# Kernel optimization log

Hardware: AMD Instinct MI355X
Metric: run time of the kernel (lower is better)

Reference implementation:

```python
import jax, jax.numpy as jnp
from jax import lax
import numpy as np

B, S, H = 8, 512, 768


def setup_inputs() -> dict:
    key = jax.random.key(0)
    ks = jax.random.split(key, 8)
    outputs = jax.random.normal(ks[0], (B, S, H), dtype=jnp.float32)
    starts = jax.random.randint(ks[1], (B,), S // 4, 3 * S // 4)
    mask = jnp.stack([starts, jnp.full((B,), S, dtype=starts.dtype)], axis=1)  # [B,2]
    sc = 1.0 / np.sqrt(H)
    Wa_w = jax.random.normal(ks[2], (H, H), dtype=jnp.float32) * sc
    Wa_b = jax.random.normal(ks[3], (H,), dtype=jnp.float32) * sc
    Ua_w = jax.random.normal(ks[4], (H, H), dtype=jnp.float32) * sc
    Ua_b = jax.random.normal(ks[5], (H,), dtype=jnp.float32) * sc
    Va_w = jax.random.normal(ks[6], (1, H), dtype=jnp.float32) * sc
    Va_b = jax.random.normal(ks[7], (1,), dtype=jnp.float32) * sc
    return {"outputs": outputs, "mask": mask, "Wa_w": Wa_w, "Wa_b": Wa_b,
            "Ua_w": Ua_w, "Ua_b": Ua_b, "Va_w": Va_w, "Va_b": Va_b}


def reference(outputs, mask, Wa_w, Wa_b, Ua_w, Ua_b, Va_w, Va_b):
    # outputs: [B,S,H]; mask[:,0] = start (source = tokens [0:start], summary = [start:S])
    b, s, h = outputs.shape
    Wq = jnp.einsum('bsh,oh->bso', outputs, Wa_w) + Wa_b  # query proj, [B,S,H]
    Uk = jnp.einsum('bsh,oh->bso', outputs, Ua_w) + Ua_b  # key proj,   [B,S,H]
    va = Va_w[0]  # [H]
    vb = Va_b[0]

    # Stream over query token positions to avoid a [B,S,S,H] tanh intermediate.
    def step(_, wq_t):  # wq_t: [B,H]
        m = jnp.tanh(wq_t[:, None, :] + Uk)          # [B,S,H]
        sc_t = jnp.einsum('bkh,h->bk', m, va) + vb   # [B,S]
        return None, sc_t

    _, scores = lax.scan(step, None, jnp.swapaxes(Wq, 0, 1))  # [S(query token), B, S(key)]
    scores = jnp.swapaxes(scores, 0, 1)  # [B, S_token, S_key]

    start = mask[:, 0]                              # [B]
    j = jnp.arange(s)
    # summary query j corresponds to token index start + j
    t_idx = jnp.clip(start[:, None] + j[None, :], 0, s - 1)            # [B,S]
    sc = jnp.take_along_axis(scores, t_idx[:, :, None], axis=1)       # [B,S,S]
    key_mask = (j[None, :] < start[:, None])                           # [B,S] valid source keys
    q_mask = (j[None, :] < (s - start)[:, None])                       # [B,S] valid summary queries

    sc = jnp.where(key_mask[:, None, :], sc, -1e30)
    w = jax.nn.softmax(sc, axis=-1)
    # zero out exactly where the torch code leaves zeros
    attentions = w * key_mask[:, None, :].astype(w.dtype) * q_mask[:, :, None].astype(w.dtype)
    contexts = jnp.einsum('bjk,bkh->bjh', attentions, outputs)
    return attentions, contexts
```

## Files before the change

### kernel.cpp

```cpp
#include <hip/hip_runtime.h>

typedef float  f32x4   __attribute__((ext_vector_type(4)));
typedef short  short8  __attribute__((ext_vector_type(8)));
typedef unsigned short ushort8 __attribute__((ext_vector_type(8)));

constexpr int kB = 8;
constexpr int kS = 512;
constexpr int kH = 768;
constexpr int kJM = 384;

constexpr float kTanhScale = 2.8853900817779268f;

__device__ __forceinline__ float native_exp2(float x) {
    float r; asm("v_exp_f32 %0, %1" : "=v"(r) : "v"(x)); return r;
}

__device__ __forceinline__ float waveMax(float v) {
#pragma unroll
    for (int off = 32; off > 0; off >>= 1) v = fmaxf(v, __shfl_xor(v, off, 64));
    return v;
}
__device__ __forceinline__ float waveSum(float v) {
#pragma unroll
    for (int off = 32; off > 0; off >>= 1) v += __shfl_xor(v, off, 64);
    return v;
}

__global__ __launch_bounds__(256) void k0_convert(
    const float* __restrict__ X, const float* __restrict__ Wa, const float* __restrict__ Ua,
    unsigned short* __restrict__ Xhi, unsigned short* __restrict__ Xlo,
    unsigned short* __restrict__ Wahi, unsigned short* __restrict__ Walo,
    unsigned short* __restrict__ Uahi, unsigned short* __restrict__ Ualo)
{
    const int i4 = blockIdx.x * 256 + threadIdx.x;
    const float* src; unsigned short *hi, *lo; int off;
    if (i4 < 786432)      { src = X;  hi = Xhi;  lo = Xlo;  off = i4; }
    else if (i4 < 933888) { src = Wa; hi = Wahi; lo = Walo; off = i4 - 786432; }
    else                  { src = Ua; hi = Uahi; lo = Ualo; off = i4 - 933888; }

    float4 v = *(const float4*)(src + (size_t)off * 4);
    unsigned short h[4], l[4];
#pragma unroll
    for (int c = 0; c < 4; ++c) {
        float x = (&v.x)[c];
        unsigned u = __float_as_uint(x);
        h[c] = (unsigned short)(u >> 16);
        float hf = __uint_as_float(u & 0xFFFF0000u);
        l[c] = (unsigned short)(__float_as_uint(x - hf) >> 16);
    }
    *(ushort4*)(hi + (size_t)off * 4) = make_ushort4(h[0], h[1], h[2], h[3]);
    *(ushort4*)(lo + (size_t)off * 4) = make_ushort4(l[0], l[1], l[2], l[3]);
}

__global__ __launch_bounds__(256) void k1_mfma(
    const unsigned short* __restrict__ Xhi, const unsigned short* __restrict__ Xlo,
    const unsigned short* __restrict__ W0hi, const unsigned short* __restrict__ W0lo,
    const unsigned short* __restrict__ W1hi, const unsigned short* __restrict__ W1lo,
    const float* __restrict__ b0, const float* __restrict__ b1,
    const int* __restrict__ mask,
    float* __restrict__ Eqc, float* __restrict__ EkTc)
{
    __shared__ char smem[49664];
    unsigned short* Ahi = (unsigned short*)smem;
    unsigned short* Alo = (unsigned short*)(smem + 10240);
    unsigned short* Bhi = (unsigned short*)(smem + 20480);
    unsigned short* Blo = (unsigned short*)(smem + 28160);

    const int z = blockIdx.z;
    const unsigned short* Whi = z ? W1hi : W0hi;
    const unsigned short* Wlo = z ? W1lo : W0lo;
    const float* bias = z ? b1 : b0;

    const int m0 = blockIdx.y * 128;
    const int n0 = blockIdx.x * 96;
    const int t  = threadIdx.x;
    const int bI = m0 >> 9;
    const int lb = m0 & (kS - 1);
    const int start = mask[2 * bI];

    if (z == 0) { if (lb + 128 <= start) return; }
    else        { if (lb >= start) return; }

    const int ar = t >> 1, ko = (t & 1) << 4;
    const bool doB = (ar < 96);
    const size_t aoff = (size_t)(m0 + ar) * kH + ko;
    const size_t woff = (size_t)(n0 + ar) * kH + ko;

    const int wid = t >> 6, lane = t & 63;
    const int wr = wid >> 1, wc = wid & 1;
    const int lr = lane & 15, lk = (lane >> 4) << 3;

    f32x4 acc[4][3];
#pragma unroll
    for (int mi = 0; mi < 4; ++mi)
#pragma unroll
        for (int ni = 0; ni < 3; ++ni)
#pragma unroll
            for (int r = 0; r < 4; ++r) acc[mi][ni][r] = 0.0f;

    for (int h0 = 0; h0 < kH; h0 += 32) {
        ushort8 ah0 = *(const ushort8*)(Xhi + aoff + h0);
        ushort8 ah1 = *(const ushort8*)(Xhi + aoff + h0 + 8);
        ushort8 al0 = *(const ushort8*)(Xlo + aoff + h0);
        ushort8 al1 = *(const ushort8*)(Xlo + aoff + h0 + 8);
        ushort8 bh0, bh1, bl0, bl1;
        if (doB) {
            bh0 = *(const ushort8*)(Whi + woff + h0);
            bh1 = *(const ushort8*)(Whi + woff + h0 + 8);
            bl0 = *(const ushort8*)(Wlo + woff + h0);
            bl1 = *(const ushort8*)(Wlo + woff + h0 + 8);
        }
        __syncthreads();
        *(ushort8*)(Ahi + ar * 40 + ko)     = ah0;
        *(ushort8*)(Ahi + ar * 40 + ko + 8) = ah1;
        *(ushort8*)(Alo + ar * 40 + ko)     = al0;
        *(ushort8*)(Alo + ar * 40 + ko + 8) = al1;
        if (doB) {
            *(ushort8*)(Bhi + ar * 40 + ko)     = bh0;
            *(ushort8*)(Bhi + ar * 40 + ko + 8) = bh1;
            *(ushort8*)(Blo + ar * 40 + ko)     = bl0;
            *(ushort8*)(Blo + ar * 40 + ko + 8) = bl1;
        }
        __syncthreads();

        short8 ah[4], al_[4], bh[3], bl[3];
#pragma unroll
        for (int mi = 0; mi < 4; ++mi) {
            const int row = wr * 64 + mi * 16 + lr;
            ah[mi]  = *(const short8*)(Ahi + row * 40 + lk);
            al_[mi] = *(const short8*)(Alo + row * 40 + lk);
        }
#pragma unroll
        for (int ni = 0; ni < 3; ++ni) {
            const int row = wc * 48 + ni * 16 + lr;
            bh[ni] = *(const short8*)(Bhi + row * 40 + lk);
            bl[ni] = *(const short8*)(Blo + row * 40 + lk);
        }
#pragma unroll
        for (int mi = 0; mi < 4; ++mi)
#pragma unroll
            for (int ni = 0; ni < 3; ++ni)
                acc[mi][ni] = __builtin_amdgcn_mfma_f32_16x16x32_bf16(ah[mi], bh[ni], acc[mi][ni], 0, 0, 0);
#pragma unroll
        for (int mi = 0; mi < 4; ++mi)
#pragma unroll
            for (int ni = 0; ni < 3; ++ni)
                acc[mi][ni] = __builtin_amdgcn_mfma_f32_16x16x32_bf16(al_[mi], bh[ni], acc[mi][ni], 0, 0, 0);
#pragma unroll
        for (int mi = 0; mi < 4; ++mi)
#pragma unroll
            for (int ni = 0; ni < 3; ++ni)
                acc[mi][ni] = __builtin_amdgcn_mfma_f32_16x16x32_bf16(ah[mi], bl[ni], acc[mi][ni], 0, 0, 0);
    }

    if (z == 0) {
#pragma unroll
        for (int mi = 0; mi < 4; ++mi)
#pragma unroll
            for (int ni = 0; ni < 3; ++ni) {
                const int ml = lb + wr * 64 + mi * 16 + ((lane >> 4) << 2);
                const int ng = n0 + wc * 48 + ni * 16 + lr;
                const float bn = bias[ng];
#pragma unroll
                for (int r = 0; r < 4; ++r) {
                    const int jj = ml + r - start;
                    if (jj >= 0)
                        Eqc[((size_t)bI * kJM + jj) * kH + ng] =
                            native_exp2((acc[mi][ni][r] + bn) * kTanhScale);
                }
            }
    } else {
        __syncthreads();
        float* stg = (float*)smem;
#pragma unroll
        for (int mi = 0; mi < 4; ++mi)
#pragma unroll
            for (int ni = 0; ni < 3; ++ni) {
                const int ml = wr * 64 + mi * 16 + ((lane >> 4) << 2);
                const int nl = wc * 48 + ni * 16 + lr;
                const float bn = bias[n0 + nl];
#pragma unroll
                for (int r = 0; r < 4; ++r)
                    stg[(ml + r) * 97 + nl] = native_exp2((acc[mi][ni][r] + bn) * kTanhScale);
            }
        __syncthreads();
        const int s4 = (t & 31) << 2, hb_ = t >> 5;
        const int sg = lb + s4;
#pragma unroll
        for (int u = 0; u < 12; ++u) {
            const int h = (u << 3) + hb_;
            float o[4] = { stg[(s4 + 0) * 97 + h], stg[(s4 + 1) * 97 + h],
                           stg[(s4 + 2) * 97 + h], stg[(s4 + 3) * 97 + h] };
            float* dst = EkTc + ((size_t)bI * kH + n0 + h) * kJM + sg;
            if (sg + 3 < start) {
                *(float4*)dst = make_float4(o[0], o[1], o[2], o[3]);
            } else {
#pragma unroll
                for (int e2 = 0; e2 < 4; ++e2)
                    if (sg + e2 < start) dst[e2] = o[e2];
            }
        }
    }
}

__global__ void k2a_worklist(const int* __restrict__ mask, int* __restrict__ wl)
{
    __shared__ int ne[kB], off[kB];
    const int tid = threadIdx.x;
    if (tid < kB) {
        int start = mask[2 * tid];
        ne[tid] = ((kS - start + 1) >> 1) * ((start + 63) >> 6) * 2;
    }
    __syncthreads();
    if (tid == 0) {
        int s = 0;
        for (int b = 0; b < kB; ++b) { off[b] = s; s += ne[b]; }
        wl[0] = s;
    }
    __syncthreads();
    for (int b = 0; b < kB; ++b) {
        int start = mask[2 * b];
        int nkw = (start + 63) >> 6;
        int n = ne[b], base = off[b];
        for (int t = tid; t < n; t += blockDim.x) {
            int c = t & 1, p = t >> 1;
            int jt = p / nkw, kt = p - jt * nkw;
            wl[1 + base + t] = (b << 16) | (jt << 8) | (kt << 1) | c;
        }
    }
}

__global__ __launch_bounds__(256) void k2_scores(
    const float* __restrict__ Eqc, const float* __restrict__ EkTc,
    const float* __restrict__ va, const int* __restrict__ mask,
    const int* __restrict__ wl, float* __restrict__ part0, float* __restrict__ part1)
{
    const int ntiles = wl[0];
    const int lane = threadIdx.x & 63;
    const int wslot = (blockIdx.x << 2) | (threadIdx.x >> 6);
    const int nslots = gridDim.x << 2;

    for (int w = wslot; w < ntiles; w += nslots) {
        const int e = __builtin_amdgcn_readfirstlane(wl[1 + w]);
        const int b = e >> 16, jt = (e >> 8) & 255, ktc = e & 255;
        const int kt = ktc >> 1, c = ktc & 1;
        const int start = __builtin_amdgcn_readfirstlane(mask[2 * b]);
        const int jmax = kS - start;
        const int j0 = jt << 1, k0 = kt << 6;
        const int hbase = c * 384;

        const float* eq0 = Eqc + ((size_t)b * kJM + j0) * kH + hbase;
        const float* eq1 = eq0 + kH;
        const float* ekp = EkTc + ((size_t)b * kH + hbase) * kJM + k0 + lane;
        const float* vap = va + hbase;

        float a0 = 0.0f, a1 = 0.0f;
        float eA[8], eB[8];
#pragma unroll
        for (int c2 = 0; c2 < 8; ++c2) eA[c2] = ekp[(size_t)c2 * kJM];
#pragma unroll
        for (int c2 = 0; c2 < 8; ++c2) eB[c2] = ekp[(size_t)(8 + c2) * kJM];

        for (int h0 = 0; h0 < 384; h0 += 16) {
            const bool more = (h0 + 16) < 384;
            float nA[8], nB[8];
            if (more) {
#pragma unroll
                for (int c2 = 0; c2 < 8; ++c2) nA[c2] = ekp[(size_t)(h0 + 16 + c2) * kJM];
            }
#pragma unroll
            for (int c2 = 0; c2 < 8; ++c2) {
                const float vc = vap[h0 + c2];
                float r0 = __builtin_amdgcn_rcpf(fmaf(eq0[h0 + c2], eA[c2], 1.0f));
                float r1 = __builtin_amdgcn_rcpf(fmaf(eq1[h0 + c2], eA[c2], 1.0f));
                a0 = fmaf(vc, r0, a0);
                a1 = fmaf(vc, r1, a1);
            }
            if (more) {
#pragma unroll
                for (int c2 = 0; c2 < 8; ++c2) nB[c2] = ekp[(size_t)(h0 + 24 + c2) * kJM];
#pragma unroll
                for (int c2 = 0; c2 < 8; ++c2) {
                    const float vc = vap[h0 + 8 + c2];
                    float r0 = __builtin_amdgcn_rcpf(fmaf(eq0[h0 + 8 + c2], eB[c2], 1.0f));
                    float r1 = __builtin_amdgcn_rcpf(fmaf(eq1[h0 + 8 + c2], eB[c2], 1.0f));
                    a0 = fmaf(vc, r0, a0);
                    a1 = fmaf(vc, r1, a1);
                }
#pragma unroll
                for (int c2 = 0; c2 < 8; ++c2) { eA[c2] = nA[c2]; eB[c2] = nB[c2]; }
            } else {
#pragma unroll
                for (int c2 = 0; c2 < 8; ++c2) {
                    const float vc = vap[h0 + 8 + c2];
                    float r0 = __builtin_amdgcn_rcpf(fmaf(eq0[h0 + 8 + c2], eB[c2], 1.0f));
                    float r1 = __builtin_amdgcn_rcpf(fmaf(eq1[h0 + 8 + c2], eB[c2], 1.0f));
                    a0 = fmaf(vc, r0, a0);
                    a1 = fmaf(vc, r1, a1);
                }
            }
        }

        float* srow = (c ? part1 : part0) + ((size_t)b * kS + j0) * kS + k0 + lane;
        if (j0 < jmax)     srow[0]  = -2.0f * a0;
        if (j0 + 1 < jmax) srow[kS] = -2.0f * a1;
    }
}

__global__ __launch_bounds__(256) void k3_softmax(
    float* __restrict__ attn, const float* __restrict__ part1,
    const int* __restrict__ mask)
{
    const int bx = blockIdx.x;
    const int b = bx >> 9;
    const int j = bx & (kS - 1);
    const int start = mask[2 * b];
    float* row = attn + ((size_t)b * kS + j) * kS;
    const int tid = threadIdx.x;

    if (j >= kS - start) {
        row[tid] = 0.0f;
        row[tid + 256] = 0.0f;
        return;
    }

    const float* p1row = part1 + ((size_t)b * kS + j) * kS;
    float v0 = (tid < start) ? row[tid] + p1row[tid] : -1e30f;
    float v1 = (tid + 256 < start) ? row[tid + 256] + p1row[tid + 256] : -1e30f;

    __shared__ float red[4];
    const int wid = tid >> 6;

    float m = waveMax(fmaxf(v0, v1));
    if ((tid & 63) == 0) red[wid] = m;
    __syncthreads();
    m = fmaxf(fmaxf(red[0], red[1]), fmaxf(red[2], red[3]));
    __syncthreads();

    float e0 = (tid < start) ? __expf(v0 - m) : 0.0f;
    float e1 = (tid + 256 < start) ? __expf(v1 - m) : 0.0f;
    float s = waveSum(e0 + e1);
    if ((tid & 63) == 0) red[wid] = s;
    __syncthreads();
    s = red[0] + red[1] + red[2] + red[3];

    float inv = __builtin_amdgcn_rcpf(s);
    row[tid] = e0 * inv;
    row[tid + 256] = e1 * inv;
}

__global__ __launch_bounds__(256) void k4_context(
    const float* __restrict__ attn, const float* __restrict__ outs,
    const int* __restrict__ mask, float* __restrict__ ctx)
{
    const int b = blockIdx.z;
    const int start = mask[2 * b];
    const int kmax = (start + 15) & ~15;
    const int m0 = blockIdx.y * 64;
    const int n0 = blockIdx.x * 64;

    __shared__ float As[16][68];
    __shared__ float Bs[16][68];

    const int tid = threadIdx.x;
    const int lrow = tid >> 2;
    const int lk4  = (tid & 3) << 2;
    const int brow = tid >> 4;
    const int bh4  = (tid & 15) << 2;
    const int is = tid >> 4;
    const int js = tid & 15;

    const float* arow = attn + ((size_t)b * kS + m0 + lrow) * kS + lk4;
    const float* bbase = outs + (size_t)b * kS * kH + n0 + bh4;

    float acc[4][4] = {};

    for (int k0 = 0; k0 < kmax; k0 += 16) {
        float4 av = *(const float4*)(arow + k0);
        float4 bv = *(const float4*)(bbase + (size_t)(k0 + brow) * kH);
        __syncthreads();
        As[lk4 + 0][lrow] = av.x;
        As[lk4 + 1][lrow] = av.y;
        As[lk4 + 2][lrow] = av.z;
        As[lk4 + 3][lrow] = av.w;
        *(float4*)&Bs[brow][bh4] = bv;
        __syncthreads();
#pragma unroll
        for (int kk = 0; kk < 16; ++kk) {
            const float* ap = &As[kk][is << 2];
            const float* bp = &Bs[kk][js << 2];
            float aa[4], bb[4];
#pragma unroll
            for (int c = 0; c < 4; ++c) { aa[c] = ap[c]; bb[c] = bp[c]; }
#pragma unroll
            for (int i = 0; i < 4; ++i)
#pragma unroll
                for (int j = 0; j < 4; ++j)
                    acc[i][j] = fmaf(aa[i], bb[j], acc[i][j]);
        }
    }

#pragma unroll
    for (int i = 0; i < 4; ++i) {
        int row = m0 + (is << 2) + i;
        float4 o = {acc[i][0], acc[i][1], acc[i][2], acc[i][3]};
        *(float4*)(ctx + ((size_t)b * kS + row) * kH + n0 + (js << 2)) = o;
    }
}

extern "C" void kernel_launch(void* const* d_in, const int* in_sizes, int n_in,
                              void* d_out, int out_size, void* d_ws, size_t ws_size,
                              hipStream_t stream)
{
    const float* outputs = (const float*)d_in[0];
    const int*   mask    = (const int*)d_in[1];
    const float* Wa_w    = (const float*)d_in[2];
    const float* Wa_b    = (const float*)d_in[3];
    const float* Ua_w    = (const float*)d_in[4];
    const float* Ua_b    = (const float*)d_in[5];
    const float* Va_w    = (const float*)d_in[6];

    float* attn = (float*)d_out;
    float* ctx  = attn + (size_t)kB * kS * kS;

    unsigned short* Xhi  = (unsigned short*)ctx;
    unsigned short* Xlo  = Xhi + (size_t)kB * kS * kH;
    unsigned short* Wahi = (unsigned short*)attn;
    unsigned short* Walo = Wahi + (size_t)kH * kH;
    unsigned short* Uahi = Walo + (size_t)kH * kH;
    unsigned short* Ualo = Uahi + (size_t)kH * kH;
    float* part1 = ctx;

    int* wl = (int*)d_ws;
    float* Eqc  = (float*)((char*)d_ws + 131072);
    float* EkTc = Eqc + (size_t)kB * kJM * kH;

    k0_convert<<<dim3(4224), 256, 0, stream>>>(
        outputs, Wa_w, Ua_w, Xhi, Xlo, Wahi, Walo, Uahi, Ualo);

    k1_mfma<<<dim3(kH / 96, (kB * kS) / 128, 2), 256, 0, stream>>>(
        Xhi, Xlo, Wahi, Walo, Uahi, Ualo, Wa_b, Ua_b, mask, Eqc, EkTc);

    k2a_worklist<<<dim3(1), 256, 0, stream>>>(mask, wl);
    k2_scores<<<dim3(2048), 256, 0, stream>>>(Eqc, EkTc, Va_w, mask, wl, attn, part1);

    k3_softmax<<<dim3(kB * kS), 256, 0, stream>>>(attn, part1, mask);

    k4_context<<<dim3(kH / 64, kS / 64, kB), 256, 0, stream>>>(attn, outputs, mask, ctx);
}
```

Before: 152.0 us.

## Drop weight lo split, inline worklist decode, and pack score math into float2

The weights are now converted to a single bfloat16 with round-to-nearest, and only the activations keep a hi/lo split. This removes a third of the MFMAs and the weight-lo loads and LDS traffic in the projection GEMM, at some cost in accuracy. The separate worklist kernel is removed; each wave decodes its tile index from per-batch offsets computed from the mask, saving one launch. The scores inner loop uses 2-wide vector FMAs so the compiler can emit packed float ops.

```diff
diff --git a/kernel.cpp b/kernel.cpp
--- a/kernel.cpp
+++ b/kernel.cpp
@@ -1,6 +1,7 @@
 #include <hip/hip_runtime.h>
 
 typedef float  f32x4   __attribute__((ext_vector_type(4)));
+typedef float  v2f     __attribute__((ext_vector_type(2)));
 typedef short  short8  __attribute__((ext_vector_type(8)));
 typedef unsigned short ushort8 __attribute__((ext_vector_type(8)));
 
@@ -15,6 +16,12 @@
     float r; asm("v_exp_f32 %0, %1" : "=v"(r) : "v"(x)); return r;
 }
 
+__device__ __forceinline__ unsigned short bf16_rtn(float x) {
+    unsigned u = __float_as_uint(x);
+    unsigned r = u + 0x7FFFu + ((u >> 16) & 1u);
+    return (unsigned short)(r >> 16);
+}
+
 __device__ __forceinline__ float waveMax(float v) {
 #pragma unroll
     for (int off = 32; off > 0; off >>= 1) v = fmaxf(v, __shfl_xor(v, off, 64));
@@ -29,33 +36,34 @@
 __global__ __launch_bounds__(256) void k0_convert(
     const float* __restrict__ X, const float* __restrict__ Wa, const float* __restrict__ Ua,
     unsigned short* __restrict__ Xhi, unsigned short* __restrict__ Xlo,
-    unsigned short* __restrict__ Wahi, unsigned short* __restrict__ Walo,
-    unsigned short* __restrict__ Uahi, unsigned short* __restrict__ Ualo)
+    unsigned short* __restrict__ Wahi, unsigned short* __restrict__ Uahi)
 {
     const int i4 = blockIdx.x * 256 + threadIdx.x;
-    const float* src; unsigned short *hi, *lo; int off;
-    if (i4 < 786432)      { src = X;  hi = Xhi;  lo = Xlo;  off = i4; }
-    else if (i4 < 933888) { src = Wa; hi = Wahi; lo = Walo; off = i4 - 786432; }
-    else                  { src = Ua; hi = Uahi; lo = Ualo; off = i4 - 933888; }
-
-    float4 v = *(const float4*)(src + (size_t)off * 4);
-    unsigned short h[4], l[4];
-#pragma unroll
-    for (int c = 0; c < 4; ++c) {
-        float x = (&v.x)[c];
-        unsigned u = __float_as_uint(x);
-        h[c] = (unsigned short)(u >> 16);
-        float hf = __uint_as_float(u & 0xFFFF0000u);
-        l[c] = (unsigned short)(__float_as_uint(x - hf) >> 16);
-    }
-    *(ushort4*)(hi + (size_t)off * 4) = make_ushort4(h[0], h[1], h[2], h[3]);
-    *(ushort4*)(lo + (size_t)off * 4) = make_ushort4(l[0], l[1], l[2], l[3]);
+    if (i4 < 786432) {
+        float4 v = *(const float4*)(X + (size_t)i4 * 4);
+        unsigned short h[4], l[4];
+#pragma unroll
+        for (int c = 0; c < 4; ++c) {
+            float x = (&v.x)[c];
+            h[c] = bf16_rtn(x);
+            float hf = __uint_as_float((unsigned)h[c] << 16);
+            l[c] = bf16_rtn(x - hf);
+        }
+        *(ushort4*)(Xhi + (size_t)i4 * 4) = make_ushort4(h[0], h[1], h[2], h[3]);
+        *(ushort4*)(Xlo + (size_t)i4 * 4) = make_ushort4(l[0], l[1], l[2], l[3]);
+    } else {
+        const float* src; unsigned short* hi; int off;
+        if (i4 < 933888) { src = Wa; hi = Wahi; off = i4 - 786432; }
+        else             { src = Ua; hi = Uahi; off = i4 - 933888; }
+        float4 v = *(const float4*)(src + (size_t)off * 4);
+        *(ushort4*)(hi + (size_t)off * 4) =
+            make_ushort4(bf16_rtn(v.x), bf16_rtn(v.y), bf16_rtn(v.z), bf16_rtn(v.w));
+    }
 }
 
 __global__ __launch_bounds__(256) void k1_mfma(
     const unsigned short* __restrict__ Xhi, const unsigned short* __restrict__ Xlo,
-    const unsigned short* __restrict__ W0hi, const unsigned short* __restrict__ W0lo,
-    const unsigned short* __restrict__ W1hi, const unsigned short* __restrict__ W1lo,
+    const unsigned short* __restrict__ W0hi, const unsigned short* __restrict__ W1hi,
     const float* __restrict__ b0, const float* __restrict__ b1,
     const int* __restrict__ mask,
     float* __restrict__ Eqc, float* __restrict__ EkTc)
@@ -64,11 +72,9 @@
     unsigned short* Ahi = (unsigned short*)smem;
     unsigned short* Alo = (unsigned short*)(smem + 10240);
     unsigned short* Bhi = (unsigned short*)(smem + 20480);
-    unsigned short* Blo = (unsigned short*)(smem + 28160);
 
     const int z = blockIdx.z;
     const unsigned short* Whi = z ? W1hi : W0hi;
-    const unsigned short* Wlo = z ? W1lo : W0lo;
     const float* bias = z ? b1 : b0;
 
     const int m0 = blockIdx.y * 128;
@@ -103,12 +109,10 @@
         ushort8 ah1 = *(const ushort8*)(Xhi + aoff + h0 + 8);
         ushort8 al0 = *(const ushort8*)(Xlo + aoff + h0);
         ushort8 al1 = *(const ushort8*)(Xlo + aoff + h0 + 8);
-        ushort8 bh0, bh1, bl0, bl1;
+        ushort8 bh0, bh1;
         if (doB) {
             bh0 = *(const ushort8*)(Whi + woff + h0);
             bh1 = *(const ushort8*)(Whi + woff + h0 + 8);
-            bl0 = *(const ushort8*)(Wlo + woff + h0);
-            bl1 = *(const ushort8*)(Wlo + woff + h0 + 8);
         }
         __syncthreads();
         *(ushort8*)(Ahi + ar * 40 + ko)     = ah0;
@@ -118,12 +122,10 @@
         if (doB) {
             *(ushort8*)(Bhi + ar * 40 + ko)     = bh0;
             *(ushort8*)(Bhi + ar * 40 + ko + 8) = bh1;
-            *(ushort8*)(Blo + ar * 40 + ko)     = bl0;
-            *(ushort8*)(Blo + ar * 40 + ko + 8) = bl1;
-        }
-        __syncthreads();
-
-        short8 ah[4], al_[4], bh[3], bl[3];
+        }
+        __syncthreads();
+
+        short8 ah[4], al_[4], bh[3];
 #pragma unroll
         for (int mi = 0; mi < 4; ++mi) {
             const int row = wr * 64 + mi * 16 + lr;
@@ -134,7 +136,6 @@
         for (int ni = 0; ni < 3; ++ni) {
             const int row = wc * 48 + ni * 16 + lr;
             bh[ni] = *(const short8*)(Bhi + row * 40 + lk);
-            bl[ni] = *(const short8*)(Blo + row * 40 + lk);
         }
 #pragma unroll
         for (int mi = 0; mi < 4; ++mi)
@@ -146,11 +147,6 @@
 #pragma unroll
             for (int ni = 0; ni < 3; ++ni)
                 acc[mi][ni] = __builtin_amdgcn_mfma_f32_16x16x32_bf16(al_[mi], bh[ni], acc[mi][ni], 0, 0, 0);
-#pragma unroll
-        for (int mi = 0; mi < 4; ++mi)
-#pragma unroll
-            for (int ni = 0; ni < 3; ++ni)
-                acc[mi][ni] = __builtin_amdgcn_mfma_f32_16x16x32_bf16(ah[mi], bl[ni], acc[mi][ni], 0, 0, 0);
     }
 
     if (z == 0) {
@@ -203,49 +199,38 @@
     }
 }
 
-__global__ void k2a_worklist(const int* __restrict__ mask, int* __restrict__ wl)
-{
-    __shared__ int ne[kB], off[kB];
-    const int tid = threadIdx.x;
-    if (tid < kB) {
-        int start = mask[2 * tid];
-        ne[tid] = ((kS - start + 1) >> 1) * ((start + 63) >> 6) * 2;
-    }
-    __syncthreads();
-    if (tid == 0) {
-        int s = 0;
-        for (int b = 0; b < kB; ++b) { off[b] = s; s += ne[b]; }
-        wl[0] = s;
-    }
-    __syncthreads();
-    for (int b = 0; b < kB; ++b) {
-        int start = mask[2 * b];
-        int nkw = (start + 63) >> 6;
-        int n = ne[b], base = off[b];
-        for (int t = tid; t < n; t += blockDim.x) {
-            int c = t & 1, p = t >> 1;
-            int jt = p / nkw, kt = p - jt * nkw;
-            wl[1 + base + t] = (b << 16) | (jt << 8) | (kt << 1) | c;
-        }
-    }
-}
-
 __global__ __launch_bounds__(256) void k2_scores(
     const float* __restrict__ Eqc, const float* __restrict__ EkTc,
     const float* __restrict__ va, const int* __restrict__ mask,
-    const int* __restrict__ wl, float* __restrict__ part0, float* __restrict__ part1)
-{
-    const int ntiles = wl[0];
+    float* __restrict__ part0, float* __restrict__ part1)
+{
     const int lane = threadIdx.x & 63;
     const int wslot = (blockIdx.x << 2) | (threadIdx.x >> 6);
     const int nslots = gridDim.x << 2;
 
+    int starts[kB], offs[kB + 1];
+    offs[0] = 0;
+#pragma unroll
+    for (int b = 0; b < kB; ++b) {
+        int s = __builtin_amdgcn_readfirstlane(mask[2 * b]);
+        starts[b] = s;
+        offs[b + 1] = offs[b] + ((kS - s + 1) >> 1) * ((s + 63) >> 6) * 2;
+    }
+    const int ntiles = offs[kB];
+    const v2f one2 = {1.0f, 1.0f};
+
     for (int w = wslot; w < ntiles; w += nslots) {
-        const int e = __builtin_amdgcn_readfirstlane(wl[1 + w]);
-        const int b = e >> 16, jt = (e >> 8) & 255, ktc = e & 255;
-        const int kt = ktc >> 1, c = ktc & 1;
-        const int start = __builtin_amdgcn_readfirstlane(mask[2 * b]);
+        int b = 0;
+#pragma unroll
+        for (int i = 1; i < kB; ++i) b += (w >= offs[i]);
+        const int start = starts[b];
         const int jmax = kS - start;
+        const int tt = w - offs[b];
+        const int c = tt & 1;
+        const int p = tt >> 1;
+        const int nkw = (start + 63) >> 6;
+        const int jt = p / nkw;
+        const int kt = p - jt * nkw;
         const int j0 = jt << 1, k0 = kt << 6;
         const int hbase = c * 384;
 
@@ -254,7 +239,7 @@
         const float* ekp = EkTc + ((size_t)b * kH + hbase) * kJM + k0 + lane;
         const float* vap = va + hbase;
 
-        float a0 = 0.0f, a1 = 0.0f;
+        v2f acc0 = {0.0f, 0.0f}, acc1 = {0.0f, 0.0f};
         float eA[8], eB[8];
 #pragma unroll
         for (int c2 = 0; c2 < 8; ++c2) eA[c2] = ekp[(size_t)c2 * kJM];
@@ -269,41 +254,44 @@
                 for (int c2 = 0; c2 < 8; ++c2) nA[c2] = ekp[(size_t)(h0 + 16 + c2) * kJM];
             }
 #pragma unroll
-            for (int c2 = 0; c2 < 8; ++c2) {
-                const float vc = vap[h0 + c2];
-                float r0 = __builtin_amdgcn_rcpf(fmaf(eq0[h0 + c2], eA[c2], 1.0f));
-                float r1 = __builtin_amdgcn_rcpf(fmaf(eq1[h0 + c2], eA[c2], 1.0f));
-                a0 = fmaf(vc, r0, a0);
-                a1 = fmaf(vc, r1, a1);
+            for (int c2 = 0; c2 < 8; c2 += 2) {
+                v2f eq0p = *(const v2f*)(eq0 + h0 + c2);
+                v2f eq1p = *(const v2f*)(eq1 + h0 + c2);
+                v2f vap2 = *(const v2f*)(vap + h0 + c2);
+                v2f ek2 = {eA[c2], eA[c2 + 1]};
+                v2f p0 = __builtin_elementwise_fma(eq0p, ek2, one2);
+                v2f p1 = __builtin_elementwise_fma(eq1p, ek2, one2);
+                v2f r0 = {__builtin_amdgcn_rcpf(p0.x), __builtin_amdgcn_rcpf(p0.y)};
+                v2f r1 = {__builtin_amdgcn_rcpf(p1.x), __builtin_amdgcn_rcpf(p1.y)};
+                acc0 = __builtin_elementwise_fma(vap2, r0, acc0);
+                acc1 = __builtin_elementwise_fma(vap2, r1, acc1);
             }
             if (more) {
 #pragma unroll
                 for (int c2 = 0; c2 < 8; ++c2) nB[c2] = ekp[(size_t)(h0 + 24 + c2) * kJM];
-#pragma unroll
-                for (int c2 = 0; c2 < 8; ++c2) {
-                    const float vc = vap[h0 + 8 + c2];
-                    float r0 = __builtin_amdgcn_rcpf(fmaf(eq0[h0 + 8 + c2], eB[c2], 1.0f));
-                    float r1 = __builtin_amdgcn_rcpf(fmaf(eq1[h0 + 8 + c2], eB[c2], 1.0f));
-                    a0 = fmaf(vc, r0, a0);
-                    a1 = fmaf(vc, r1, a1);
-                }
+            }
+#pragma unroll
+            for (int c2 = 0; c2 < 8; c2 += 2) {
+                v2f eq0p = *(const v2f*)(eq0 + h0 + 8 + c2);
+                v2f eq1p = *(const v2f*)(eq1 + h0 + 8 + c2);
+                v2f vap2 = *(const v2f*)(vap + h0 + 8 + c2);
+                v2f ek2 = {eB[c2], eB[c2 + 1]};
+                v2f p0 = __builtin_elementwise_fma(eq0p, ek2, one2);
+                v2f p1 = __builtin_elementwise_fma(eq1p, ek2, one2);
+                v2f r0 = {__builtin_amdgcn_rcpf(p0.x), __builtin_amdgcn_rcpf(p0.y)};
+                v2f r1 = {__builtin_amdgcn_rcpf(p1.x), __builtin_amdgcn_rcpf(p1.y)};
+                acc0 = __builtin_elementwise_fma(vap2, r0, acc0);
+                acc1 = __builtin_elementwise_fma(vap2, r1, acc1);
+            }
+            if (more) {
 #pragma unroll
                 for (int c2 = 0; c2 < 8; ++c2) { eA[c2] = nA[c2]; eB[c2] = nB[c2]; }
-            } else {
-#pragma unroll
-                for (int c2 = 0; c2 < 8; ++c2) {
-                    const float vc = vap[h0 + 8 + c2];
-                    float r0 = __builtin_amdgcn_rcpf(fmaf(eq0[h0 + 8 + c2], eB[c2], 1.0f));
-                    float r1 = __builtin_amdgcn_rcpf(fmaf(eq1[h0 + 8 + c2], eB[c2], 1.0f));
-                    a0 = fmaf(vc, r0, a0);
-                    a1 = fmaf(vc, r1, a1);
-                }
             }
         }
 
         float* srow = (c ? part1 : part0) + ((size_t)b * kS + j0) * kS + k0 + lane;
-        if (j0 < jmax)     srow[0]  = -2.0f * a0;
-        if (j0 + 1 < jmax) srow[kS] = -2.0f * a1;
+        if (j0 < jmax)     srow[0]  = -2.0f * (acc0.x + acc0.y);
+        if (j0 + 1 < jmax) srow[kS] = -2.0f * (acc1.x + acc1.y);
     }
 }
 
@@ -426,23 +414,19 @@
     unsigned short* Xhi  = (unsigned short*)ctx;
     unsigned short* Xlo  = Xhi + (size_t)kB * kS * kH;
     unsigned short* Wahi = (unsigned short*)attn;
-    unsigned short* Walo = Wahi + (size_t)kH * kH;
-    unsigned short* Uahi = Walo + (size_t)kH * kH;
-    unsigned short* Ualo = Uahi + (size_t)kH * kH;
+    unsigned short* Uahi = Wahi + (size_t)kH * kH;
     float* part1 = ctx;
 
-    int* wl = (int*)d_ws;
-    float* Eqc  = (float*)((char*)d_ws + 131072);
+    float* Eqc  = (float*)d_ws;
     float* EkTc = Eqc + (size_t)kB * kJM * kH;
 
     k0_convert<<<dim3(4224), 256, 0, stream>>>(
-        outputs, Wa_w, Ua_w, Xhi, Xlo, Wahi, Walo, Uahi, Ualo);
+        outputs, Wa_w, Ua_w, Xhi, Xlo, Wahi, Uahi);
 
     k1_mfma<<<dim3(kH / 96, (kB * kS) / 128, 2), 256, 0, stream>>>(
-        Xhi, Xlo, Wahi, Walo, Uahi, Ualo, Wa_b, Ua_b, mask, Eqc, EkTc);
-
-    k2a_worklist<<<dim3(1), 256, 0, stream>>>(mask, wl);
-    k2_scores<<<dim3(2048), 256, 0, stream>>>(Eqc, EkTc, Va_w, mask, wl, attn, part1);
+        Xhi, Xlo, Wahi, Uahi, Wa_b, Ua_b, mask, Eqc, EkTc);
+
+    k2_scores<<<dim3(2048), 256, 0, stream>>>(Eqc, EkTc, Va_w, mask, attn, part1);
 
     k3_softmax<<<dim3(kB * kS), 256, 0, stream>>>(attn, part1, mask);
 
```

Result: slower. 180.2 us (+18.6%).
